# Kernel optimization log

Hardware: AMD Instinct MI355X
Metric: run time of the kernel (lower is better)

The kernel has to match this reference:

```python
import jax, jax.numpy as jnp
import numpy as np

DIM = 64
N_ENTITY = 1000000
N_RELATION = 32
L = 2
B = 4096
K = 64


def setup_inputs() -> dict:
    key = jax.random.key(0)
    ks = jax.random.split(key, 24)
    s = 0.05
    d = DIM
    inp = {
        "items": jax.random.randint(ks[0], (B,), 0, N_ENTITY),
        "heads": jax.random.randint(ks[1], (L, B, K), 0, N_ENTITY),
        "relations": jax.random.randint(ks[2], (L, B, K), 0, N_RELATION),
        "tails": jax.random.randint(ks[3], (L, B, K), 0, N_ENTITY),
        # learned parameters
        "embedding": jax.random.normal(ks[4], (N_ENTITY, d), jnp.float32) * s,
        "transformer": jax.random.normal(ks[5], (N_RELATION, d), jnp.float32) * s,
        "attn_w": jax.random.normal(ks[6], (1, 3 * d), jnp.float32) * s,
        "attn_b": jax.random.normal(ks[7], (1,), jnp.float32) * s,
        "W_ih": jax.random.normal(ks[8], (d, d), jnp.float32) * s,
        "W_hh": jax.random.normal(ks[9], (d, d), jnp.float32) * s,
        "b_ih": jax.random.normal(ks[10], (d,), jnp.float32) * s,
        "b_hh": jax.random.normal(ks[11], (d,), jnp.float32) * s,
        "l1_w": jax.random.normal(ks[12], (d, 2 * d), jnp.float32) * s,
        "l1_b": jax.random.normal(ks[13], (d,), jnp.float32) * s,
        "l2_w": jax.random.normal(ks[14], (d, d), jnp.float32) * s,
        "l2_b": jax.random.normal(ks[15], (d,), jnp.float32) * s,
        "l3_w": jax.random.normal(ks[16], (d, d), jnp.float32) * s,
        "l3_b": jax.random.normal(ks[17], (d,), jnp.float32) * s,
        "lin_w": jax.random.normal(ks[18], (1, 2 * d), jnp.float32) * s,
        "lin_b": jax.random.normal(ks[19], (1,), jnp.float32) * s,
    }
    return inp


def _ncfg_forward(embedding, transformer, attn_w, attn_b, W_ih, W_hh, b_ih, b_hh,
                  l1_w, l1_b, l2_w, l2_b, l3_w, l3_b, lin_w, lin_b,
                  items, heads, relations, tails):
    o_sum = jnp.zeros((B, DIM), embedding.dtype)
    for l in range(L):
        h = embedding[heads[l]]          # [B, K, d]
        r = transformer[relations[l]]    # [B, K, d]
        tl = embedding[tails[l]]         # [B, K, d]
        hRt = jnp.concatenate([h, r, tl], axis=-1)                  # [B, K, 3d]
        pi = jax.nn.sigmoid(hRt @ attn_w.T + attn_b)                # [B, K, 1]
        pi = jax.nn.softmax(pi, axis=1)                             # softmax over neighbors
        # 2-step tanh RNN over seq (head, tail), h0 = 0
        h1 = jnp.tanh(h @ W_ih.T + b_ih + b_hh)                     # [B, K, d]
        h2 = jnp.tanh(tl @ W_ih.T + b_ih + h1 @ W_hh.T + b_hh)      # [B, K, d]
        o_sum = o_sum + (pi * h2).sum(axis=1)                       # [B, d]
    user_emb = o_sum
    item_emb = embedding[items]                                     # [B, d]
    # NCF head (dropout in eval mode = identity)
    ui = jnp.concatenate([user_emb, item_emb], axis=-1)             # [B, 2d]
    y = jax.nn.relu(ui @ l1_w.T + l1_b)
    y = jax.nn.relu(y @ l2_w.T + l2_b)
    y1 = jax.nn.sigmoid(y @ l3_w.T + l3_b)
    y2 = user_emb * item_emb
    out = jax.nn.sigmoid(jnp.concatenate([y1, y2], axis=-1) @ lin_w.T + lin_b)
    return out[:, 0]  # squeeze -> [B]


def reference(items, heads, relations, tails, embedding, transformer, attn_w, attn_b,
              W_ih, W_hh, b_ih, b_hh, l1_w, l1_b, l2_w, l2_b, l3_w, l3_b, lin_w, lin_b):
    return _ncfg_forward(embedding, transformer, attn_w, attn_b, W_ih, W_hh, b_ih, b_hh,
                         l1_w, l1_b, l2_w, l2_b, l3_w, l3_b, lin_w, lin_b,
                         items, heads, relations, tails)
```

## Files before the change

kernel.cpp:

```cpp
#include <hip/hip_runtime.h>
#include <hip/hip_bf16.h>
#include <cstdint>
#include <cstddef>

#define B_SZ 4096
#define STRIDE 72

typedef __attribute__((ext_vector_type(4))) float f32x4;
typedef __attribute__((ext_vector_type(8))) short sv8;
typedef __attribute__((ext_vector_type(8))) __bf16 bfv8;

__device__ __align__(16) short g_wf[2][8][64][8];
__device__ float g_bsum[64];
__device__ float g_reldot[32];

static __device__ __forceinline__ short f2bf(float x) {
  union { float f; unsigned u; } v; v.f = x;
  unsigned r = v.u + 0x7fffu + ((v.u >> 16) & 1u);
  return (short)(r >> 16);
}

static __device__ __forceinline__ f32x4 MFMA(sv8 a, sv8 b, f32x4 c) {
  return __builtin_amdgcn_mfma_f32_16x16x32_bf16(
      __builtin_bit_cast(bfv8, a), __builtin_bit_cast(bfv8, b), c, 0, 0, 0);
}

static __device__ __forceinline__ float fast_sigmoid(float x) {
  return __builtin_amdgcn_rcpf(1.f + __expf(-x));
}
static __device__ __forceinline__ float fast_tanh(float x) {
  const float e = __expf(2.f * x);
  return 1.f - 2.f * __builtin_amdgcn_rcpf(e + 1.f);
}
static __device__ __forceinline__ float dot4(f32x4 a, f32x4 b) {
  return a.x * b.x + a.y * b.y + a.z * b.z + a.w * b.w;
}
static __device__ __forceinline__ sv8 pack8(f32x4 a, f32x4 b) {
  sv8 f;
  f[0] = f2bf(a.x); f[1] = f2bf(a.y); f[2] = f2bf(a.z); f[3] = f2bf(a.w);
  f[4] = f2bf(b.x); f[5] = f2bf(b.y); f[6] = f2bf(b.z); f[7] = f2bf(b.w);
  return f;
}

__global__ __launch_bounds__(256) void ncfg_prep(
    const float* __restrict__ W_ih, const float* __restrict__ W_hh,
    const float* __restrict__ b_ih, const float* __restrict__ b_hh,
    const float* __restrict__ trf, const float* __restrict__ attn_w) {
  const int t = threadIdx.x;
  for (int q = t; q < 1024; q += 256) {
    const int m = q >> 9, f = (q >> 6) & 7, ln = q & 63;
    const int nt = f >> 1, kh = f & 1, fr = ln & 15, fg = ln >> 4;
    const float* W = m ? W_hh : W_ih;
    const float* src = W + (nt * 16 + fr) * 64 + kh * 32 + fg * 8;
    short* dst = &g_wf[m][f][ln][0];
    #pragma unroll
    for (int j = 0; j < 8; ++j) dst[j] = f2bf(src[j]);
  }
  if (t < 64) g_bsum[t] = b_ih[t] + b_hh[t];
  if (t < 32) {
    float s = 0.f;
    #pragma unroll 8
    for (int c = 0; c < 64; ++c) s += trf[t * 64 + c] * attn_w[64 + c];
    g_reldot[t] = s;
  }
}

__global__ __launch_bounds__(256, 4) void ncfg_neigh(
    const int* __restrict__ heads, const int* __restrict__ rels,
    const int* __restrict__ tails, const float* __restrict__ emb,
    const float* __restrict__ attn_w, const float* __restrict__ attn_b,
    float* __restrict__ opart) {
  const int bid = blockIdx.x;
  const int layer = bid >> 12;
  const int b = bid & (B_SZ - 1);
  const int t = threadIdx.x;
  const int lane = t & 63;
  const int w = t >> 6;
  const int fr = lane & 15;
  const int fg = lane >> 4;

  __shared__ __align__(16) short h1_bf[64 * STRIDE];
  __shared__ float logits[64];
  __shared__ float pi_s[64];
  __shared__ float o_lds[4][64];

  const int row = (w << 4) + fr;
  const size_t ibase = ((size_t)layer * B_SZ + b) * 64;
  const int hi = heads[ibase + row];
  const int ti = tails[ibase + row];
  const int ri = rels[ibase + row];

  const float* hrow = emb + (size_t)hi * 64;
  const float* trow = emb + (size_t)ti * 64;
  const int c0 = fg * 8;
  const f32x4 h0a = *(const f32x4*)(hrow + c0);
  const f32x4 h0b = *(const f32x4*)(hrow + c0 + 4);
  const f32x4 h1a = *(const f32x4*)(hrow + 32 + c0);
  const f32x4 h1b = *(const f32x4*)(hrow + 32 + c0 + 4);
  const f32x4 t0a = *(const f32x4*)(trow + c0);
  const f32x4 t0b = *(const f32x4*)(trow + c0 + 4);
  const f32x4 t1a = *(const f32x4*)(trow + 32 + c0);
  const f32x4 t1b = *(const f32x4*)(trow + 32 + c0 + 4);

  sv8 wih[8];
  #pragma unroll
  for (int f = 0; f < 8; ++f) wih[f] = *(const sv8*)&g_wf[0][f][lane][0];
  float bsum[4];
  #pragma unroll
  for (int nt = 0; nt < 4; ++nt) bsum[nt] = g_bsum[nt * 16 + fr];

  const f32x4 ah0a = *(const f32x4*)(attn_w + c0);
  const f32x4 ah0b = *(const f32x4*)(attn_w + c0 + 4);
  const f32x4 ah1a = *(const f32x4*)(attn_w + 32 + c0);
  const f32x4 ah1b = *(const f32x4*)(attn_w + 32 + c0 + 4);
  const f32x4 at0a = *(const f32x4*)(attn_w + 128 + c0);
  const f32x4 at0b = *(const f32x4*)(attn_w + 128 + c0 + 4);
  const f32x4 at1a = *(const f32x4*)(attn_w + 160 + c0);
  const f32x4 at1b = *(const f32x4*)(attn_w + 160 + c0 + 4);
  float ap = dot4(h0a, ah0a) + dot4(h0b, ah0b) + dot4(h1a, ah1a) +
             dot4(h1b, ah1b) + dot4(t0a, at0a) + dot4(t0b, at0b) +
             dot4(t1a, at1a) + dot4(t1b, at1b);
  ap += __shfl_xor(ap, 16);
  ap += __shfl_xor(ap, 32);
  if (fg == 0) logits[row] = ap + g_reldot[ri];

  sv8 ha[2], ta[2];
  ha[0] = pack8(h0a, h0b);
  ha[1] = pack8(h1a, h1b);
  ta[0] = pack8(t0a, t0b);
  ta[1] = pack8(t1a, t1b);

  __syncthreads();

  if (w == 0) {
    const float x = logits[lane] + attn_b[0];
    const float s = fast_sigmoid(x);
    float mx = s;
    #pragma unroll
    for (int m = 1; m < 64; m <<= 1) mx = fmaxf(mx, __shfl_xor(mx, m));
    const float e = __expf(s - mx);
    float sm = e;
    #pragma unroll
    for (int m = 1; m < 64; m <<= 1) sm += __shfl_xor(sm, m);
    pi_s[lane] = e * __builtin_amdgcn_rcpf(sm);
  }

  const f32x4 zz = {0.f, 0.f, 0.f, 0.f};

  f32x4 acc[4] = {zz, zz, zz, zz};
  #pragma unroll
  for (int kh = 0; kh < 2; ++kh)
    #pragma unroll
    for (int nt = 0; nt < 4; ++nt) acc[nt] = MFMA(ha[kh], wih[nt * 2 + kh], acc[nt]);

  sv8 whh[8];
  #pragma unroll
  for (int f = 0; f < 8; ++f) whh[f] = *(const sv8*)&g_wf[1][f][lane][0];

  #pragma unroll
  for (int nt = 0; nt < 4; ++nt)
    #pragma unroll
    for (int r = 0; r < 4; ++r)
      h1_bf[((w << 4) + (fg << 2) + r) * STRIDE + nt * 16 + fr] =
          f2bf(fast_tanh(acc[nt][r] + bsum[nt]));

  f32x4 acc2[4] = {zz, zz, zz, zz};
  #pragma unroll
  for (int kh = 0; kh < 2; ++kh)
    #pragma unroll
    for (int nt = 0; nt < 4; ++nt) acc2[nt] = MFMA(ta[kh], wih[nt * 2 + kh], acc2[nt]);
  const int arow = ((w << 4) + fr) * STRIDE;
  #pragma unroll
  for (int kh = 0; kh < 2; ++kh) {
    const sv8 a = *(const sv8*)&h1_bf[arow + kh * 32 + fg * 8];
    #pragma unroll
    for (int nt = 0; nt < 4; ++nt) acc2[nt] = MFMA(a, whh[nt * 2 + kh], acc2[nt]);
  }

  __syncthreads();

  const f32x4 piv = *(const f32x4*)&pi_s[(w << 4) + (fg << 2)];
  #pragma unroll
  for (int nt = 0; nt < 4; ++nt) {
    float s = piv.x * fast_tanh(acc2[nt][0] + bsum[nt]) +
              piv.y * fast_tanh(acc2[nt][1] + bsum[nt]) +
              piv.z * fast_tanh(acc2[nt][2] + bsum[nt]) +
              piv.w * fast_tanh(acc2[nt][3] + bsum[nt]);
    s += __shfl_xor(s, 16);
    s += __shfl_xor(s, 32);
    if (lane < 16) o_lds[w][nt * 16 + fr] = s;
  }
  __syncthreads();
  if (w == 0) {
    const float o =
        o_lds[0][lane] + o_lds[1][lane] + o_lds[2][lane] + o_lds[3][lane];
    opart[((size_t)layer * B_SZ + b) * 64 + lane] = o;
  }
}

__global__ __launch_bounds__(256) void ncfg_head(
    const float* __restrict__ opart, const float* __restrict__ emb,
    const int* __restrict__ items, const float* __restrict__ l1_w,
    const float* __restrict__ l1_b, const float* __restrict__ l2_w,
    const float* __restrict__ l2_b, const float* __restrict__ l3_w,
    const float* __restrict__ l3_b, const float* __restrict__ lin_w,
    const float* __restrict__ lin_b, float* __restrict__ out) {
  const int wv = threadIdx.x >> 6;
  const int i = threadIdx.x & 63;
  const int b = blockIdx.x * 4 + wv;

  __shared__ float ui[4][128];
  __shared__ float yy[4][64];

  const float ue = opart[(size_t)b * 64 + i] +
                   opart[((size_t)B_SZ + b) * 64 + i];
  const float ie = emb[(size_t)items[b] * 64 + i];
  ui[wv][i] = ue;
  ui[wv][64 + i] = ie;
  __syncthreads();

  float acc = l1_b[i];
  {
    const float* wr = l1_w + i * 128;
    #pragma unroll
    for (int j = 0; j < 128; j += 4) {
      const f32x4 wvv = *(const f32x4*)(wr + j);
      const f32x4 uv = *(const f32x4*)&ui[wv][j];
      acc += wvv.x * uv.x + wvv.y * uv.y + wvv.z * uv.z + wvv.w * uv.w;
    }
  }
  float y = fmaxf(acc, 0.f);
  yy[wv][i] = y;
  __syncthreads();

  acc = l2_b[i];
  {
    const float* wr = l2_w + i * 64;
    #pragma unroll
    for (int j = 0; j < 64; j += 4) {
      const f32x4 wvv = *(const f32x4*)(wr + j);
      const f32x4 uv = *(const f32x4*)&yy[wv][j];
      acc += wvv.x * uv.x + wvv.y * uv.y + wvv.z * uv.z + wvv.w * uv.w;
    }
  }
  y = fmaxf(acc, 0.f);
  __syncthreads();
  yy[wv][i] = y;
  __syncthreads();

  acc = l3_b[i];
  {
    const float* wr = l3_w + i * 64;
    #pragma unroll
    for (int j = 0; j < 64; j += 4) {
      const f32x4 wvv = *(const f32x4*)(wr + j);
      const f32x4 uv = *(const f32x4*)&yy[wv][j];
      acc += wvv.x * uv.x + wvv.y * uv.y + wvv.z * uv.z + wvv.w * uv.w;
    }
  }
  const float y1 = fast_sigmoid(acc);
  const float y2 = ue * ie;

  float part = y1 * lin_w[i] + y2 * lin_w[64 + i];
  #pragma unroll
  for (int m = 1; m < 64; m <<= 1) part += __shfl_xor(part, m);
  if (i == 0) out[b] = fast_sigmoid(part + lin_b[0]);
}

extern "C" void kernel_launch(void* const* d_in, const int* in_sizes, int n_in,
                              void* d_out, int out_size, void* d_ws,
                              size_t ws_size, hipStream_t stream) {
  (void)in_sizes; (void)n_in; (void)out_size; (void)ws_size;
  const int* items = (const int*)d_in[0];
  const int* heads = (const int*)d_in[1];
  const int* rels = (const int*)d_in[2];
  const int* tails = (const int*)d_in[3];
  const float* emb = (const float*)d_in[4];
  const float* trf = (const float*)d_in[5];
  const float* attn_w = (const float*)d_in[6];
  const float* attn_b = (const float*)d_in[7];
  const float* W_ih = (const float*)d_in[8];
  const float* W_hh = (const float*)d_in[9];
  const float* b_ih = (const float*)d_in[10];
  const float* b_hh = (const float*)d_in[11];
  const float* l1_w = (const float*)d_in[12];
  const float* l1_b = (const float*)d_in[13];
  const float* l2_w = (const float*)d_in[14];
  const float* l2_b = (const float*)d_in[15];
  const float* l3_w = (const float*)d_in[16];
  const float* l3_b = (const float*)d_in[17];
  const float* lin_w = (const float*)d_in[18];
  const float* lin_b = (const float*)d_in[19];
  float* out = (float*)d_out;
  float* opart = (float*)d_ws;

  ncfg_prep<<<dim3(1), dim3(256), 0, stream>>>(W_ih, W_hh, b_ih, b_hh, trf,
                                               attn_w);
  ncfg_neigh<<<dim3(2 * B_SZ), dim3(256), 0, stream>>>(
      heads, rels, tails, emb, attn_w, attn_b, opart);
  ncfg_head<<<dim3(B_SZ / 4), dim3(256), 0, stream>>>(
      opart, emb, items, l1_w, l1_b, l2_w, l2_b, l3_w, l3_b, lin_w, lin_b,
      out);
}
```

Baseline: 103.1 us.

## Map one wave per (layer,batch) item with chunked loop and online softmax

Each wave now processes a full (layer, batch) item by looping over four 16-row neighbor chunks, instead of a 256-thread block handling one item. The block-wide barriers and LDS reductions go away, and softmax normalization is deferred. The attention logits are now computed with an MFMA against a prepacked bf16 attention-weight fragment rather than scalar dot products. The sigmoid output lies in (0,1), so exp is taken without max-subtraction. Each wave keeps more registers live, so the occupancy hint drops to 3, and the per-wave serial loop may expose gather latency.

```diff
diff --git a/kernel.cpp b/kernel.cpp
--- a/kernel.cpp
+++ b/kernel.cpp
@@ -4,13 +4,13 @@
 #include <cstddef>
 
 #define B_SZ 4096
-#define STRIDE 72
 
 typedef __attribute__((ext_vector_type(4))) float f32x4;
 typedef __attribute__((ext_vector_type(8))) short sv8;
 typedef __attribute__((ext_vector_type(8))) __bf16 bfv8;
 
 __device__ __align__(16) short g_wf[2][8][64][8];
+__device__ __align__(16) short g_af[2][2][64][8];
 __device__ float g_bsum[64];
 __device__ float g_reldot[32];
 
@@ -31,9 +31,6 @@
 static __device__ __forceinline__ float fast_tanh(float x) {
   const float e = __expf(2.f * x);
   return 1.f - 2.f * __builtin_amdgcn_rcpf(e + 1.f);
-}
-static __device__ __forceinline__ float dot4(f32x4 a, f32x4 b) {
-  return a.x * b.x + a.y * b.y + a.z * b.z + a.w * b.w;
 }
 static __device__ __forceinline__ sv8 pack8(f32x4 a, f32x4 b) {
   sv8 f;
@@ -56,6 +53,14 @@
     #pragma unroll
     for (int j = 0; j < 8; ++j) dst[j] = f2bf(src[j]);
   }
+  {
+    const int a = t >> 7, kh = (t >> 6) & 1, ln = t & 63;
+    const int n = ln & 15, kf = ln >> 4;
+    short* dst = &g_af[a][kh][ln][0];
+    #pragma unroll
+    for (int j = 0; j < 8; ++j)
+      dst[j] = (n == 0) ? f2bf(attn_w[a * 128 + kh * 32 + kf * 8 + j]) : (short)0;
+  }
   if (t < 64) g_bsum[t] = b_ih[t] + b_hh[t];
   if (t < 32) {
     float s = 0.f;
@@ -65,136 +70,140 @@
   }
 }
 
-__global__ __launch_bounds__(256, 4) void ncfg_neigh(
+__global__ __launch_bounds__(256, 3) void ncfg_neigh(
     const int* __restrict__ heads, const int* __restrict__ rels,
     const int* __restrict__ tails, const float* __restrict__ emb,
-    const float* __restrict__ attn_w, const float* __restrict__ attn_b,
-    float* __restrict__ opart) {
-  const int bid = blockIdx.x;
-  const int layer = bid >> 12;
-  const int b = bid & (B_SZ - 1);
+    const float* __restrict__ attn_b, float* __restrict__ opart) {
   const int t = threadIdx.x;
   const int lane = t & 63;
   const int w = t >> 6;
+  const int item = blockIdx.x * 4 + w;
   const int fr = lane & 15;
   const int fg = lane >> 4;
-
-  __shared__ __align__(16) short h1_bf[64 * STRIDE];
-  __shared__ float logits[64];
-  __shared__ float pi_s[64];
-  __shared__ float o_lds[4][64];
-
-  const int row = (w << 4) + fr;
-  const size_t ibase = ((size_t)layer * B_SZ + b) * 64;
-  const int hi = heads[ibase + row];
-  const int ti = tails[ibase + row];
-  const int ri = rels[ibase + row];
-
-  const float* hrow = emb + (size_t)hi * 64;
-  const float* trow = emb + (size_t)ti * 64;
   const int c0 = fg * 8;
-  const f32x4 h0a = *(const f32x4*)(hrow + c0);
-  const f32x4 h0b = *(const f32x4*)(hrow + c0 + 4);
-  const f32x4 h1a = *(const f32x4*)(hrow + 32 + c0);
-  const f32x4 h1b = *(const f32x4*)(hrow + 32 + c0 + 4);
-  const f32x4 t0a = *(const f32x4*)(trow + c0);
-  const f32x4 t0b = *(const f32x4*)(trow + c0 + 4);
-  const f32x4 t1a = *(const f32x4*)(trow + 32 + c0);
-  const f32x4 t1b = *(const f32x4*)(trow + 32 + c0 + 4);
-
-  sv8 wih[8];
+
+  __shared__ __align__(16) short h1s[4][16 * 72];
+  __shared__ __align__(16) float e_s[4][16];
+
+  const size_t ibase = (size_t)item * 64;
+  int hiA[4], tiA[4], riA[4];
+  #pragma unroll
+  for (int c = 0; c < 4; ++c) {
+    hiA[c] = heads[ibase + c * 16 + fr];
+    tiA[c] = tails[ibase + c * 16 + fr];
+    riA[c] = rels[ibase + c * 16 + fr];
+  }
+
+  sv8 wih[8], whh[8], abf[4];
   #pragma unroll
   for (int f = 0; f < 8; ++f) wih[f] = *(const sv8*)&g_wf[0][f][lane][0];
+  #pragma unroll
+  for (int f = 0; f < 8; ++f) whh[f] = *(const sv8*)&g_wf[1][f][lane][0];
+  abf[0] = *(const sv8*)&g_af[0][0][lane][0];
+  abf[1] = *(const sv8*)&g_af[0][1][lane][0];
+  abf[2] = *(const sv8*)&g_af[1][0][lane][0];
+  abf[3] = *(const sv8*)&g_af[1][1][lane][0];
   float bsum[4];
   #pragma unroll
   for (int nt = 0; nt < 4; ++nt) bsum[nt] = g_bsum[nt * 16 + fr];
-
-  const f32x4 ah0a = *(const f32x4*)(attn_w + c0);
-  const f32x4 ah0b = *(const f32x4*)(attn_w + c0 + 4);
-  const f32x4 ah1a = *(const f32x4*)(attn_w + 32 + c0);
-  const f32x4 ah1b = *(const f32x4*)(attn_w + 32 + c0 + 4);
-  const f32x4 at0a = *(const f32x4*)(attn_w + 128 + c0);
-  const f32x4 at0b = *(const f32x4*)(attn_w + 128 + c0 + 4);
-  const f32x4 at1a = *(const f32x4*)(attn_w + 160 + c0);
-  const f32x4 at1b = *(const f32x4*)(attn_w + 160 + c0 + 4);
-  float ap = dot4(h0a, ah0a) + dot4(h0b, ah0b) + dot4(h1a, ah1a) +
-             dot4(h1b, ah1b) + dot4(t0a, at0a) + dot4(t0b, at0b) +
-             dot4(t1a, at1a) + dot4(t1b, at1b);
-  ap += __shfl_xor(ap, 16);
-  ap += __shfl_xor(ap, 32);
-  if (fg == 0) logits[row] = ap + g_reldot[ri];
-
-  sv8 ha[2], ta[2];
-  ha[0] = pack8(h0a, h0b);
-  ha[1] = pack8(h1a, h1b);
-  ta[0] = pack8(t0a, t0b);
-  ta[1] = pack8(t1a, t1b);
-
-  __syncthreads();
-
-  if (w == 0) {
-    const float x = logits[lane] + attn_b[0];
-    const float s = fast_sigmoid(x);
-    float mx = s;
-    #pragma unroll
-    for (int m = 1; m < 64; m <<= 1) mx = fmaxf(mx, __shfl_xor(mx, m));
-    const float e = __expf(s - mx);
-    float sm = e;
-    #pragma unroll
-    for (int m = 1; m < 64; m <<= 1) sm += __shfl_xor(sm, m);
-    pi_s[lane] = e * __builtin_amdgcn_rcpf(sm);
-  }
+  const float ab0 = attn_b[0];
 
   const f32x4 zz = {0.f, 0.f, 0.f, 0.f};
-
-  f32x4 acc[4] = {zz, zz, zz, zz};
-  #pragma unroll
-  for (int kh = 0; kh < 2; ++kh)
-    #pragma unroll
-    for (int nt = 0; nt < 4; ++nt) acc[nt] = MFMA(ha[kh], wih[nt * 2 + kh], acc[nt]);
-
-  sv8 whh[8];
-  #pragma unroll
-  for (int f = 0; f < 8; ++f) whh[f] = *(const sv8*)&g_wf[1][f][lane][0];
-
-  #pragma unroll
-  for (int nt = 0; nt < 4; ++nt)
-    #pragma unroll
-    for (int r = 0; r < 4; ++r)
-      h1_bf[((w << 4) + (fg << 2) + r) * STRIDE + nt * 16 + fr] =
-          f2bf(fast_tanh(acc[nt][r] + bsum[nt]));
-
-  f32x4 acc2[4] = {zz, zz, zz, zz};
-  #pragma unroll
-  for (int kh = 0; kh < 2; ++kh)
-    #pragma unroll
-    for (int nt = 0; nt < 4; ++nt) acc2[nt] = MFMA(ta[kh], wih[nt * 2 + kh], acc2[nt]);
-  const int arow = ((w << 4) + fr) * STRIDE;
-  #pragma unroll
-  for (int kh = 0; kh < 2; ++kh) {
-    const sv8 a = *(const sv8*)&h1_bf[arow + kh * 32 + fg * 8];
-    #pragma unroll
-    for (int nt = 0; nt < 4; ++nt) acc2[nt] = MFMA(a, whh[nt * 2 + kh], acc2[nt]);
-  }
-
-  __syncthreads();
-
-  const f32x4 piv = *(const f32x4*)&pi_s[(w << 4) + (fg << 2)];
+  f32x4 o_acc[4] = {zz, zz, zz, zz};
+  float se = 0.f;
+
+  #pragma unroll
+  for (int c = 0; c < 4; ++c) {
+    const float* hr = emb + (size_t)hiA[c] * 64;
+    const float* tr = emb + (size_t)tiA[c] * 64;
+    const f32x4 h0 = *(const f32x4*)(hr + c0);
+    const f32x4 h1 = *(const f32x4*)(hr + c0 + 4);
+    const f32x4 h2 = *(const f32x4*)(hr + 32 + c0);
+    const f32x4 h3 = *(const f32x4*)(hr + 32 + c0 + 4);
+    const f32x4 t0 = *(const f32x4*)(tr + c0);
+    const f32x4 t1 = *(const f32x4*)(tr + c0 + 4);
+    const f32x4 t2 = *(const f32x4*)(tr + 32 + c0);
+    const f32x4 t3 = *(const f32x4*)(tr + 32 + c0 + 4);
+
+    const sv8 ha0 = pack8(h0, h1), ha1 = pack8(h2, h3);
+    const sv8 ta0 = pack8(t0, t1), ta1 = pack8(t2, t3);
+
+    f32x4 accl = zz;
+    accl = MFMA(ha0, abf[0], accl);
+    accl = MFMA(ha1, abf[1], accl);
+    accl = MFMA(ta0, abf[2], accl);
+    accl = MFMA(ta1, abf[3], accl);
+
+    float ev4[4];
+    #pragma unroll
+    for (int r = 0; r < 4; ++r) {
+      const int rr = __shfl(riA[c], fg * 4 + r);
+      const float x = accl[r] + g_reldot[rr] + ab0;
+      ev4[r] = __expf(fast_sigmoid(x));
+    }
+    if (fr == 0) {
+      f32x4 evv = {ev4[0], ev4[1], ev4[2], ev4[3]};
+      *(f32x4*)&e_s[w][fg * 4] = evv;
+    }
+    const f32x4 ev = *(const f32x4*)&e_s[w][fg * 4];
+    {
+      float loc = ev.x + ev.y + ev.z + ev.w;
+      loc += __shfl_xor(loc, 16);
+      loc += __shfl_xor(loc, 32);
+      se += loc;
+    }
+
+    f32x4 acc[4] = {zz, zz, zz, zz};
+    #pragma unroll
+    for (int nt = 0; nt < 4; ++nt) acc[nt] = MFMA(ha0, wih[nt * 2], acc[nt]);
+    #pragma unroll
+    for (int nt = 0; nt < 4; ++nt) acc[nt] = MFMA(ha1, wih[nt * 2 + 1], acc[nt]);
+    #pragma unroll
+    for (int nt = 0; nt < 4; ++nt)
+      #pragma unroll
+      for (int r = 0; r < 4; ++r)
+        h1s[w][(fg * 4 + r) * 72 + nt * 16 + fr] =
+            f2bf(fast_tanh(acc[nt][r] + bsum[nt]));
+
+    f32x4 acc2[4] = {zz, zz, zz, zz};
+    #pragma unroll
+    for (int nt = 0; nt < 4; ++nt) acc2[nt] = MFMA(ta0, wih[nt * 2], acc2[nt]);
+    #pragma unroll
+    for (int nt = 0; nt < 4; ++nt) acc2[nt] = MFMA(ta1, wih[nt * 2 + 1], acc2[nt]);
+    const sv8 a1 = *(const sv8*)&h1s[w][fr * 72 + c0];
+    const sv8 a2 = *(const sv8*)&h1s[w][fr * 72 + 32 + c0];
+    #pragma unroll
+    for (int nt = 0; nt < 4; ++nt) acc2[nt] = MFMA(a1, whh[nt * 2], acc2[nt]);
+    #pragma unroll
+    for (int nt = 0; nt < 4; ++nt) acc2[nt] = MFMA(a2, whh[nt * 2 + 1], acc2[nt]);
+
+    #pragma unroll
+    for (int nt = 0; nt < 4; ++nt) {
+      f32x4 th;
+      th.x = ev.x * fast_tanh(acc2[nt][0] + bsum[nt]);
+      th.y = ev.y * fast_tanh(acc2[nt][1] + bsum[nt]);
+      th.z = ev.z * fast_tanh(acc2[nt][2] + bsum[nt]);
+      th.w = ev.w * fast_tanh(acc2[nt][3] + bsum[nt]);
+      o_acc[nt] += th;
+    }
+  }
+
+  float inv;
+  {
+    inv = __builtin_amdgcn_rcpf(se);
+  }
+  float o[4];
   #pragma unroll
   for (int nt = 0; nt < 4; ++nt) {
-    float s = piv.x * fast_tanh(acc2[nt][0] + bsum[nt]) +
-              piv.y * fast_tanh(acc2[nt][1] + bsum[nt]) +
-              piv.z * fast_tanh(acc2[nt][2] + bsum[nt]) +
-              piv.w * fast_tanh(acc2[nt][3] + bsum[nt]);
+    float s = o_acc[nt].x + o_acc[nt].y + o_acc[nt].z + o_acc[nt].w;
     s += __shfl_xor(s, 16);
     s += __shfl_xor(s, 32);
-    if (lane < 16) o_lds[w][nt * 16 + fr] = s;
-  }
-  __syncthreads();
-  if (w == 0) {
-    const float o =
-        o_lds[0][lane] + o_lds[1][lane] + o_lds[2][lane] + o_lds[3][lane];
-    opart[((size_t)layer * B_SZ + b) * 64 + lane] = o;
+    o[nt] = s * inv;
+  }
+  if (fg == 0) {
+    #pragma unroll
+    for (int nt = 0; nt < 4; ++nt)
+      opart[ibase + nt * 16 + fr] = o[nt];
   }
 }
 
@@ -296,8 +305,8 @@
 
   ncfg_prep<<<dim3(1), dim3(256), 0, stream>>>(W_ih, W_hh, b_ih, b_hh, trf,
                                                attn_w);
-  ncfg_neigh<<<dim3(2 * B_SZ), dim3(256), 0, stream>>>(
-      heads, rels, tails, emb, attn_w, attn_b, opart);
+  ncfg_neigh<<<dim3(2 * B_SZ / 4), dim3(256), 0, stream>>>(
+      heads, rels, tails, emb, attn_b, opart);
   ncfg_head<<<dim3(B_SZ / 4), dim3(256), 0, stream>>>(
       opart, emb, items, l1_w, l1_b, l2_w, l2_b, l3_w, l3_b, lin_w, lin_b,
       out);
```

Result: slower. 140.7 us (+36.5%).
